# Performance work log

Hardware: AMD Instinct MI355X
Metric: run time of the kernel (lower is better)

The kernel has to match this reference:

```python
import jax, jax.numpy as jnp
import numpy as np

NX, NY, NZ = 432, 496, 1
C = 64            # num_bev_features
B = 8             # batch size
P_PER_B = 16000   # pillars per sample


def setup_inputs() -> dict:
    key = jax.random.key(0)
    kf, kp = jax.random.split(key)
    pillar_features = jax.random.normal(kf, (B * P_PER_B, C), dtype=jnp.float32)
    # unique linear (y*NX + x) indices per batch element -> deterministic scatter
    keys = jax.random.split(kp, B)
    lin = jax.vmap(lambda k: jax.random.permutation(k, NY * NX)[:P_PER_B])(keys)  # [B, P_PER_B]
    lin = lin.reshape(-1).astype(jnp.int64)
    batch_ids = jnp.repeat(jnp.arange(B, dtype=jnp.int64), P_PER_B)
    z = jnp.zeros_like(batch_ids)
    y = lin // NX
    x = lin % NX
    coords = jnp.stack([batch_ids, z, y, x], axis=1)  # [P, 4] (batch, z, y, x)
    return {"pillar_features": pillar_features, "coords": coords, "batch_size": B}


def reference(pillar_features, coords, batch_size):
    # Fused scatter replacing the per-batch python loop:
    # per-batch linear index = z + y*NX + x (nz==1 so z==0), offset by batch*NY*NX.
    lin = coords[:, 1] + coords[:, 2] * NX + coords[:, 3]
    gidx = coords[:, 0] * (NZ * NY * NX) + lin  # [P] global index
    flat = jnp.zeros((batch_size * NZ * NY * NX, pillar_features.shape[1]),
                     dtype=pillar_features.dtype)
    flat = flat.at[gidx].set(pillar_features)          # [B*ny*nx, C]
    bev = flat.reshape(batch_size, NY, NX, -1)         # [B, ny, nx, C]
    return jnp.transpose(bev, (0, 3, 1, 2))            # [B, C, ny, nx]
```

## Files before the change

### kernel.cpp

```cpp
#include <hip/hip_runtime.h>


#define PX_NX 432
#define PX_NY 496
#define PX_C 64
#define PX_NYX (PX_NY * PX_NX)
#define CSPLIT 4

typedef float floatx4 __attribute__((ext_vector_type(4)));
typedef long longx4 __attribute__((ext_vector_type(4)));

__global__ void pps_init_map(int4* __restrict__ map4, int n4) {
    int i = blockIdx.x * blockDim.x + threadIdx.x;
    if (i < n4) {
        map4[i] = make_int4(-1, -1, -1, -1);
    }
    if (blockIdx.x == 0 && threadIdx.x < 16) {
        map4[n4 + threadIdx.x] = make_int4(0, 0, 0, 0);
    }
}

__global__ void pps_detect_dtype(const int* __restrict__ c32,
                                 int* __restrict__ flag) {
    if (blockIdx.x == 0 && threadIdx.x == 0) {
        int nz = 0;
#pragma unroll
        for (int p = 0; p < 16; ++p) nz |= c32[4 * p + 3];
        *flag = (nz == 0) ? 1 : 0;
    }
}

__global__ void pps_scatter_ids(const int* __restrict__ c32,
                                const longx4* __restrict__ c64,
                                const int* __restrict__ flag,
                                int* __restrict__ map, int P, int map_n) {
    int p = blockIdx.x * blockDim.x + threadIdx.x;
    if (p >= P) return;
    long g;
    if (*flag) {
        longx4 cv = c64[p];
        g = cv.x * PX_NYX + cv.y + cv.z * PX_NX + cv.w;
    } else {
        int4 cv = ((const int4*)c32)[p];
        g = (long)cv.x * PX_NYX + (long)cv.y + (long)cv.z * PX_NX + (long)cv.w;
    }
    if (g >= 0 && g < (long)map_n) map[(int)g] = p;
}

__global__ void pps_gather(const float* __restrict__ feat,
                           const int* __restrict__ map,
                           const float* __restrict__ zrow,
                           float* __restrict__ out, int total) {
    int i = blockIdx.x * blockDim.x + threadIdx.x;
    if (i >= total) return;

    const int xq = PX_NX / 4;
    int x4 = i % xq;
    int t = i / xq;
    int y = t % PX_NY;
    int t2 = t / PX_NY;
    int b = t2 % 8;
    int cs = t2 / 8;

    int sbase = b * PX_NYX + y * PX_NX + x4 * 4;
    int4 pid = ((const int4*)map)[sbase >> 2];

    const float* r0 = (pid.x >= 0) ? feat + (size_t)pid.x * PX_C : zrow;
    const float* r1 = (pid.y >= 0) ? feat + (size_t)pid.y * PX_C : zrow;
    const float* r2 = (pid.z >= 0) ? feat + (size_t)pid.z * PX_C : zrow;
    const float* r3 = (pid.w >= 0) ? feat + (size_t)pid.w * PX_C : zrow;

    const int c_lo = cs * (PX_C / CSPLIT);
    float* ob = out + (size_t)b * ((size_t)PX_C * PX_NYX)
                    + (size_t)y * PX_NX + (size_t)x4 * 4;

#pragma unroll
    for (int cc = 0; cc < (PX_C / CSPLIT) / 4; ++cc) {
        int c0 = c_lo + cc * 4;
        floatx4 q0 = *(const floatx4*)(r0 + c0);
        floatx4 q1 = *(const floatx4*)(r1 + c0);
        floatx4 q2 = *(const floatx4*)(r2 + c0);
        floatx4 q3 = *(const floatx4*)(r3 + c0);
#pragma unroll
        for (int k = 0; k < 4; ++k) {
            floatx4 v;
            v.x = q0[k];
            v.y = q1[k];
            v.z = q2[k];
            v.w = q3[k];
            __builtin_nontemporal_store(
                v, (floatx4*)(ob + (size_t)(c0 + k) * PX_NYX));
        }
    }
}

extern "C" void kernel_launch(void* const* d_in, const int* in_sizes, int n_in,
                              void* d_out, int out_size, void* d_ws, size_t ws_size,
                              hipStream_t stream) {
    const float* feat = (const float*)d_in[0];
    const int* coords32 = (const int*)d_in[1];
    const longx4* coords64 = (const longx4*)d_in[1];
    float* out = (float*)d_out;
    int* map = (int*)d_ws;

    int B = out_size / (PX_C * PX_NYX);
    int P = in_sizes[1] / 4;

    int map_n = B * PX_NYX;
    int map_n4 = map_n / 4;
    const float* zrow = (const float*)(map + map_n);
    int* flag = map + map_n + 64;

    int total = B * PX_NY * (PX_NX / 4) * CSPLIT;

    pps_init_map<<<(map_n4 + 255) / 256, 256, 0, stream>>>((int4*)map, map_n4);
    pps_detect_dtype<<<1, 64, 0, stream>>>(coords32, flag);
    pps_scatter_ids<<<(P + 255) / 256, 256, 0, stream>>>(
        coords32, coords64, flag, map, P, map_n);
    pps_gather<<<(total + 255) / 256, 256, 0, stream>>>(feat, map, zrow, out, total);
}
```

Before: 463.1 us.

## Fuse map init, scatter and gather into one cooperative persistent kernel

Replaces four separate kernel launches (map init, dtype detect, id scatter, gather) with a single cooperative kernel of 1024 blocks that uses grid-stride loops and grid.sync() between phases. This removes the launch overhead and inter-kernel gaps. In exchange it adds two grid-wide barriers and limits the gather to a fixed persistent grid, which may lower memory-level parallelism for the large output write. The launch also relies on all 1024 blocks fitting co-resident.

```diff
diff --git a/kernel.cpp b/kernel.cpp
--- a/kernel.cpp
+++ b/kernel.cpp
@@ -1,4 +1,7 @@
 #include <hip/hip_runtime.h>
+#include <hip/hip_cooperative_groups.h>
+
+namespace cg = cooperative_groups;
 
 
 #define PX_NX 432
@@ -6,90 +9,90 @@
 #define PX_C 64
 #define PX_NYX (PX_NY * PX_NX)
 #define CSPLIT 4
+#define GRID_BLOCKS 1024
+#define BLOCK_THREADS 256
 
 typedef float floatx4 __attribute__((ext_vector_type(4)));
 typedef long longx4 __attribute__((ext_vector_type(4)));
 
-__global__ void pps_init_map(int4* __restrict__ map4, int n4) {
-    int i = blockIdx.x * blockDim.x + threadIdx.x;
-    if (i < n4) {
-        map4[i] = make_int4(-1, -1, -1, -1);
-    }
-    if (blockIdx.x == 0 && threadIdx.x < 16) {
-        map4[n4 + threadIdx.x] = make_int4(0, 0, 0, 0);
-    }
-}
+__global__ __launch_bounds__(BLOCK_THREADS, 4) void pps_fused(
+    const float* __restrict__ feat,
+    const int* __restrict__ c32,
+    const longx4* __restrict__ c64,
+    int* __restrict__ map,
+    float* __restrict__ zrow,
+    int* __restrict__ flagp,
+    float* __restrict__ out,
+    int P, int map_n, int total) {
+    cg::grid_group grid = cg::this_grid();
+    const int gid = blockIdx.x * blockDim.x + threadIdx.x;
+    const int gsz = GRID_BLOCKS * BLOCK_THREADS;
 
-__global__ void pps_detect_dtype(const int* __restrict__ c32,
-                                 int* __restrict__ flag) {
-    if (blockIdx.x == 0 && threadIdx.x == 0) {
+    int4* map4 = (int4*)map;
+    const int n4 = map_n >> 2;
+    for (int i = gid; i < n4; i += gsz) map4[i] = make_int4(-1, -1, -1, -1);
+    if (gid < 64) zrow[gid] = 0.0f;
+    if (gid == 0) {
         int nz = 0;
 #pragma unroll
         for (int p = 0; p < 16; ++p) nz |= c32[4 * p + 3];
-        *flag = (nz == 0) ? 1 : 0;
+        *flagp = (nz == 0) ? 1 : 0;
     }
-}
+    grid.sync();
 
-__global__ void pps_scatter_ids(const int* __restrict__ c32,
-                                const longx4* __restrict__ c64,
-                                const int* __restrict__ flag,
-                                int* __restrict__ map, int P, int map_n) {
-    int p = blockIdx.x * blockDim.x + threadIdx.x;
-    if (p >= P) return;
-    long g;
-    if (*flag) {
-        longx4 cv = c64[p];
-        g = cv.x * PX_NYX + cv.y + cv.z * PX_NX + cv.w;
-    } else {
-        int4 cv = ((const int4*)c32)[p];
-        g = (long)cv.x * PX_NYX + (long)cv.y + (long)cv.z * PX_NX + (long)cv.w;
+    const int flag = *flagp;
+    for (int p = gid; p < P; p += gsz) {
+        long g;
+        if (flag) {
+            longx4 cv = c64[p];
+            g = cv.x * PX_NYX + cv.y + cv.z * PX_NX + cv.w;
+        } else {
+            int4 cv = ((const int4*)c32)[p];
+            g = (long)cv.x * PX_NYX + (long)cv.y + (long)cv.z * PX_NX
+                + (long)cv.w;
+        }
+        if (g >= 0 && g < (long)map_n) map[(int)g] = p;
     }
-    if (g >= 0 && g < (long)map_n) map[(int)g] = p;
-}
+    grid.sync();
 
-__global__ void pps_gather(const float* __restrict__ feat,
-                           const int* __restrict__ map,
-                           const float* __restrict__ zrow,
-                           float* __restrict__ out, int total) {
-    int i = blockIdx.x * blockDim.x + threadIdx.x;
-    if (i >= total) return;
+    for (int i = gid; i < total; i += gsz) {
+        const int xq = PX_NX / 4;
+        int x4 = i % xq;
+        int t = i / xq;
+        int y = t % PX_NY;
+        int t2 = t / PX_NY;
+        int b = t2 % 8;
+        int cs = t2 / 8;
 
-    const int xq = PX_NX / 4;
-    int x4 = i % xq;
-    int t = i / xq;
-    int y = t % PX_NY;
-    int t2 = t / PX_NY;
-    int b = t2 % 8;
-    int cs = t2 / 8;
+        int sbase = b * PX_NYX + y * PX_NX + x4 * 4;
+        int4 pid = ((const int4*)map)[sbase >> 2];
 
-    int sbase = b * PX_NYX + y * PX_NX + x4 * 4;
-    int4 pid = ((const int4*)map)[sbase >> 2];
+        const float* r0 = (pid.x >= 0) ? feat + (size_t)pid.x * PX_C : zrow;
+        const float* r1 = (pid.y >= 0) ? feat + (size_t)pid.y * PX_C : zrow;
+        const float* r2 = (pid.z >= 0) ? feat + (size_t)pid.z * PX_C : zrow;
+        const float* r3 = (pid.w >= 0) ? feat + (size_t)pid.w * PX_C : zrow;
 
-    const float* r0 = (pid.x >= 0) ? feat + (size_t)pid.x * PX_C : zrow;
-    const float* r1 = (pid.y >= 0) ? feat + (size_t)pid.y * PX_C : zrow;
-    const float* r2 = (pid.z >= 0) ? feat + (size_t)pid.z * PX_C : zrow;
-    const float* r3 = (pid.w >= 0) ? feat + (size_t)pid.w * PX_C : zrow;
-
-    const int c_lo = cs * (PX_C / CSPLIT);
-    float* ob = out + (size_t)b * ((size_t)PX_C * PX_NYX)
-                    + (size_t)y * PX_NX + (size_t)x4 * 4;
+        const int c_lo = cs * (PX_C / CSPLIT);
+        float* ob = out + (size_t)b * ((size_t)PX_C * PX_NYX)
+                        + (size_t)y * PX_NX + (size_t)x4 * 4;
 
 #pragma unroll
-    for (int cc = 0; cc < (PX_C / CSPLIT) / 4; ++cc) {
-        int c0 = c_lo + cc * 4;
-        floatx4 q0 = *(const floatx4*)(r0 + c0);
-        floatx4 q1 = *(const floatx4*)(r1 + c0);
-        floatx4 q2 = *(const floatx4*)(r2 + c0);
-        floatx4 q3 = *(const floatx4*)(r3 + c0);
+        for (int cc = 0; cc < 4; ++cc) {
+            int c0 = c_lo + cc * 4;
+            floatx4 q0 = *(const floatx4*)(r0 + c0);
+            floatx4 q1 = *(const floatx4*)(r1 + c0);
+            floatx4 q2 = *(const floatx4*)(r2 + c0);
+            floatx4 q3 = *(const floatx4*)(r3 + c0);
 #pragma unroll
-        for (int k = 0; k < 4; ++k) {
-            floatx4 v;
-            v.x = q0[k];
-            v.y = q1[k];
-            v.z = q2[k];
-            v.w = q3[k];
-            __builtin_nontemporal_store(
-                v, (floatx4*)(ob + (size_t)(c0 + k) * PX_NYX));
+            for (int k = 0; k < 4; ++k) {
+                floatx4 v;
+                v.x = q0[k];
+                v.y = q1[k];
+                v.z = q2[k];
+                v.w = q3[k];
+                __builtin_nontemporal_store(
+                    v, (floatx4*)(ob + (size_t)(c0 + k) * PX_NYX));
+            }
         }
     }
 }
@@ -98,8 +101,8 @@
                               void* d_out, int out_size, void* d_ws, size_t ws_size,
                               hipStream_t stream) {
     const float* feat = (const float*)d_in[0];
-    const int* coords32 = (const int*)d_in[1];
-    const longx4* coords64 = (const longx4*)d_in[1];
+    const int* c32 = (const int*)d_in[1];
+    const longx4* c64 = (const longx4*)d_in[1];
     float* out = (float*)d_out;
     int* map = (int*)d_ws;
 
@@ -107,15 +110,14 @@
     int P = in_sizes[1] / 4;
 
     int map_n = B * PX_NYX;
-    int map_n4 = map_n / 4;
-    const float* zrow = (const float*)(map + map_n);
-    int* flag = map + map_n + 64;
+    float* zrow = (float*)(map + map_n);
+    int* flagp = map + map_n + 64;
 
     int total = B * PX_NY * (PX_NX / 4) * CSPLIT;
 
-    pps_init_map<<<(map_n4 + 255) / 256, 256, 0, stream>>>((int4*)map, map_n4);
-    pps_detect_dtype<<<1, 64, 0, stream>>>(coords32, flag);
-    pps_scatter_ids<<<(P + 255) / 256, 256, 0, stream>>>(
-        coords32, coords64, flag, map, P, map_n);
-    pps_gather<<<(total + 255) / 256, 256, 0, stream>>>(feat, map, zrow, out, total);
+    void* args[] = {(void*)&feat, (void*)&c32, (void*)&c64, (void*)&map,
+                    (void*)&zrow, (void*)&flagp, (void*)&out,
+                    (void*)&P, (void*)&map_n, (void*)&total};
+    hipLaunchCooperativeKernel((const void*)pps_fused, dim3(GRID_BLOCKS),
+                               dim3(BLOCK_THREADS), args, 0, stream);
 }
```

Result: slower. 626.5 us (+35.3%).
